# Kernel optimization log

Hardware: AMD Instinct MI355X
Metric: run time of the kernel (lower is better)

## Reference

```python
import jax, jax.numpy as jnp
import numpy as np
from jax.scipy.linalg import expm

DIM = 1024


def setup_inputs() -> dict:
    key = jax.random.key(0)
    k1, k2 = jax.random.split(key)
    x = jax.random.normal(k1, (4, 4096, DIM), dtype=jnp.float32)
    skew_weights = jax.random.normal(k2, (DIM, DIM), dtype=jnp.float32) * 0.01
    return {"x": x, "skew_weights": skew_weights}


def reference(x, skew_weights):
    # A is skew-symmetric -> expm(A) is a rotation in SO(dim)
    A = skew_weights - skew_weights.T          # [dim, dim]
    R = expm(A)                                # [dim, dim]
    return jnp.matmul(x, R)                    # [..., dim] @ [dim, dim]
```

## Files before the change

kernel.cpp:

```cpp
#include <hip/hip_runtime.h>
#include <stdint.h>

#define DIM 1024
#define GLOBAL_AS __attribute__((address_space(1)))
#define LDS_AS __attribute__((address_space(3)))

typedef short bf16x8 __attribute__((ext_vector_type(8)));
typedef float f32x4 __attribute__((ext_vector_type(4)));

#define C3 0.16666667f
#define C4 0.041666668f
#define C5 0.008333334f
#define C6 0.0013888889f
#define C7 1.9841270e-4f
#define C8 2.4801587e-5f

__device__ __forceinline__ unsigned short f32_to_bf16(float f) {
    union { float f; uint32_t u; } v; v.f = f;
    uint32_t u = v.u;
    u += 0x7FFFu + ((u >> 16) & 1u);
    return (unsigned short)(u >> 16);
}
__device__ __forceinline__ float bf16_to_f32(unsigned short u) {
    union { uint32_t u; float f; } v; v.u = ((uint32_t)u) << 16;
    return v.f;
}

__device__ __forceinline__ void async16(const void* g, void* l) {
    __builtin_amdgcn_global_load_lds((GLOBAL_AS const void*)g,
                                     (LDS_AS void*)l, 16, 0, 0);
}

__global__ __launch_bounds__(256) void k_init(const float* __restrict__ W,
        unsigned short* __restrict__ Ab, unsigned short* __restrict__ G) {
    int idx = blockIdx.x * 256 + threadIdx.x;
    int i = idx >> 10, j = idx & 1023;
    float a = W[i * DIM + j] - W[j * DIM + i];
    Ab[idx] = f32_to_bf16(a);
    G[idx]  = f32_to_bf16(-a);
}

__global__ __launch_bounds__(256) void k_convert(const float* __restrict__ X,
        unsigned short* __restrict__ Xb) {
    int id = blockIdx.x * 256 + threadIdx.x;
    const f32x4* p = (const f32x4*)(X + (size_t)id * 8);
    f32x4 v0 = p[0], v1 = p[1];
    unsigned short o[8];
    #pragma unroll
    for (int q = 0; q < 4; q++) { o[q] = f32_to_bf16(v0[q]); o[4 + q] = f32_to_bf16(v1[q]); }
    *(bf16x8*)&Xb[(size_t)id * 8] = *(bf16x8*)o;
}

template<int MODE>
__global__ __launch_bounds__(256) void k_pgemm(
        const unsigned short* __restrict__ P,
        const unsigned short* __restrict__ Qt,
        const unsigned short* __restrict__ Ab,
        const unsigned short* __restrict__ A2b,
        unsigned short* __restrict__ out1,
        unsigned short* __restrict__ out2) {
    __shared__ unsigned short lP[64 * 256];
    __shared__ unsigned short lQ[64 * 256];
    int tid = threadIdx.x;
    int m0 = blockIdx.y * 64, n0 = blockIdx.x * 64;
    int lane = tid & 63, w = tid >> 6;
    int wr = w >> 1, wc = w & 1;
    int rr = lane & 15, ko = lane >> 4;
    f32x4 acc[2][2] = {};
    for (int ks = 0; ks < 4; ks++) {
        int kb = ks * 256;
        #pragma unroll
        for (int i = 0; i < 8; i++) {
            int l = i * 256 + tid;
            int r = l >> 5, cst = l & 31;
            int cd = cst ^ (r & 7);
            async16(&P[(m0 + r) * DIM + kb + cd * 8], &lP[l * 8]);
            async16(&Qt[(n0 + r) * DIM + kb + cd * 8], &lQ[l * 8]);
        }
        __syncthreads();
        #pragma unroll
        for (int s = 0; s < 8; s++) {
            int cd = s * 4 + ko;
            bf16x8 af[2], bq[2];
            #pragma unroll
            for (int mi = 0; mi < 2; mi++) {
                int ra = wr * 32 + mi * 16 + rr;
                af[mi] = *(const bf16x8*)&lP[ra * 256 + ((cd ^ (ra & 7)) * 8)];
            }
            #pragma unroll
            for (int ni = 0; ni < 2; ni++) {
                int rb = wc * 32 + ni * 16 + rr;
                bq[ni] = *(const bf16x8*)&lQ[rb * 256 + ((cd ^ (rb & 7)) * 8)];
            }
            #pragma unroll
            for (int mi = 0; mi < 2; mi++)
                #pragma unroll
                for (int ni = 0; ni < 2; ni++)
                    acc[mi][ni] = __builtin_amdgcn_mfma_f32_16x16x32_bf16(
                        af[mi], bq[ni], acc[mi][ni], 0, 0, 0);
        }
        __syncthreads();
    }
    if (MODE == 1 || MODE == 2) {
        #pragma unroll
        for (int mi = 0; mi < 2; mi++)
            #pragma unroll
            for (int ni = 0; ni < 2; ni++)
                #pragma unroll
                for (int q = 0; q < 4; q++) {
                    int rl = wr * 32 + mi * 16 + ko * 4 + q;
                    int cl = wc * 32 + ni * 16 + rr;
                    int gi = (m0 + rl) * DIM + n0 + cl;
                    float v = acc[mi][ni][q];
                    out1[gi] = f32_to_bf16(v);
                    if (MODE == 1) {
                        float a = bf16_to_f32(Ab[gi]);
                        float d = (m0 + rl == n0 + cl) ? C6 : 0.0f;
                        out2[gi] = f32_to_bf16(d - C7 * a + C8 * v);
                    }
                }
    } else {
        float* tb = (float*)lP;
        #pragma unroll
        for (int mi = 0; mi < 2; mi++)
            #pragma unroll
            for (int ni = 0; ni < 2; ni++)
                #pragma unroll
                for (int q = 0; q < 4; q++) {
                    int rl = wr * 32 + mi * 16 + ko * 4 + q;
                    int cl = wc * 32 + ni * 16 + rr;
                    int gi = (m0 + rl) * DIM + n0 + cl;
                    float a = bf16_to_f32(Ab[gi]);
                    float a2 = bf16_to_f32(A2b[gi]);
                    float d = (m0 + rl == n0 + cl) ? 1.0f : 0.0f;
                    float v;
                    if (MODE == 3) v = acc[mi][ni][q] + C3 * d + C4 * a + C5 * a2;
                    else           v = acc[mi][ni][q] + d + a + 0.5f * a2;
                    tb[cl * 65 + rl] = v;
                }
        __syncthreads();
        #pragma unroll
        for (int q = 0; q < 16; q++) {
            int l = tid * 16 + q;
            int orow = l >> 6, ocol = l & 63;
            out1[(n0 + orow) * DIM + m0 + ocol] = f32_to_bf16(tb[orow * 65 + ocol]);
        }
    }
}

__global__ __launch_bounds__(256) void k_biggemm(
        const unsigned short* __restrict__ Xb,
        const unsigned short* __restrict__ Rtb,
        float* __restrict__ Out) {
    __shared__ unsigned short lX[128 * 32];
    __shared__ unsigned short lB[256 * 32];
    int tid = threadIdx.x;
    int bid = blockIdx.x;
    int m0 = (bid & 127) * 128, n0 = (bid >> 7) * 256;
    int lane = tid & 63, w = tid >> 6;
    int wr = w >> 1, wc = w & 1;
    int rr = lane & 15, ko = lane >> 4;
    f32x4 acc[4][8] = {};
    for (int kb = 0; kb < DIM; kb += 32) {
        #pragma unroll
        for (int i = 0; i < 2; i++) {
            int l = i * 256 + tid;
            int r = l >> 2, cst = l & 3;
            int cd = cst ^ ((r >> 1) & 3);
            async16(&Xb[(m0 + r) * DIM + kb + cd * 8], &lX[l * 8]);
        }
        #pragma unroll
        for (int i = 0; i < 4; i++) {
            int l = i * 256 + tid;
            int r = l >> 2, cst = l & 3;
            int cd = cst ^ ((r >> 1) & 3);
            async16(&Rtb[(n0 + r) * DIM + kb + cd * 8], &lB[l * 8]);
        }
        __syncthreads();
        bf16x8 af[4], bq[8];
        #pragma unroll
        for (int mi = 0; mi < 4; mi++) {
            int ra = wr * 64 + mi * 16 + rr;
            af[mi] = *(const bf16x8*)&lX[ra * 32 + ((ko ^ ((ra >> 1) & 3)) * 8)];
        }
        #pragma unroll
        for (int ni = 0; ni < 8; ni++) {
            int rb = wc * 128 + ni * 16 + rr;
            bq[ni] = *(const bf16x8*)&lB[rb * 32 + ((ko ^ ((rb >> 1) & 3)) * 8)];
        }
        #pragma unroll
        for (int mi = 0; mi < 4; mi++)
            #pragma unroll
            for (int ni = 0; ni < 8; ni++)
                acc[mi][ni] = __builtin_amdgcn_mfma_f32_16x16x32_bf16(
                    af[mi], bq[ni], acc[mi][ni], 0, 0, 0);
        __syncthreads();
    }
    #pragma unroll
    for (int mi = 0; mi < 4; mi++)
        #pragma unroll
        for (int ni = 0; ni < 8; ni++)
            #pragma unroll
            for (int q = 0; q < 4; q++) {
                int row = m0 + wr * 64 + mi * 16 + ko * 4 + q;
                int col = n0 + wc * 128 + ni * 16 + rr;
                Out[(size_t)row * DIM + col] = acc[mi][ni][q];
            }
}

__global__ __launch_bounds__(256) void k_biggemm_cvt(
        const float* __restrict__ X,
        const unsigned short* __restrict__ Rtb,
        float* __restrict__ Out) {
    __shared__ unsigned short lX[128 * 32];
    __shared__ unsigned short lB[256 * 32];
    int tid = threadIdx.x;
    int bid = blockIdx.x;
    int m0 = (bid & 127) * 128, n0 = (bid >> 7) * 256;
    int lane = tid & 63, w = tid >> 6;
    int wr = w >> 1, wc = w & 1;
    int rr = lane & 15, ko = lane >> 4;
    f32x4 acc[4][8] = {};
    int xr = tid >> 1, xh = tid & 1;
    int q3 = (xr >> 1) & 3;
    for (int kb = 0; kb < DIM; kb += 32) {
        {
            const float* xp = &X[(size_t)(m0 + xr) * DIM + kb + xh * 16];
            float xv[16];
            *(f32x4*)&xv[0] = *(const f32x4*)&xp[0];
            *(f32x4*)&xv[4] = *(const f32x4*)&xp[4];
            *(f32x4*)&xv[8] = *(const f32x4*)&xp[8];
            *(f32x4*)&xv[12] = *(const f32x4*)&xp[12];
            unsigned short xs[16];
            #pragma unroll
            for (int q = 0; q < 16; q++) xs[q] = f32_to_bf16(xv[q]);
            *(bf16x8*)&lX[xr * 32 + (((2 * xh) ^ q3) * 8)]     = *(bf16x8*)&xs[0];
            *(bf16x8*)&lX[xr * 32 + (((2 * xh + 1) ^ q3) * 8)] = *(bf16x8*)&xs[8];
        }
        #pragma unroll
        for (int i = 0; i < 4; i++) {
            int l = i * 256 + tid;
            int r = l >> 2, cst = l & 3;
            int cd = cst ^ ((r >> 1) & 3);
            async16(&Rtb[(n0 + r) * DIM + kb + cd * 8], &lB[l * 8]);
        }
        __syncthreads();
        bf16x8 af[4], bq[8];
        #pragma unroll
        for (int mi = 0; mi < 4; mi++) {
            int ra = wr * 64 + mi * 16 + rr;
            af[mi] = *(const bf16x8*)&lX[ra * 32 + ((ko ^ ((ra >> 1) & 3)) * 8)];
        }
        #pragma unroll
        for (int ni = 0; ni < 8; ni++) {
            int rb = wc * 128 + ni * 16 + rr;
            bq[ni] = *(const bf16x8*)&lB[rb * 32 + ((ko ^ ((rb >> 1) & 3)) * 8)];
        }
        #pragma unroll
        for (int mi = 0; mi < 4; mi++)
            #pragma unroll
            for (int ni = 0; ni < 8; ni++)
                acc[mi][ni] = __builtin_amdgcn_mfma_f32_16x16x32_bf16(
                    af[mi], bq[ni], acc[mi][ni], 0, 0, 0);
        __syncthreads();
    }
    #pragma unroll
    for (int mi = 0; mi < 4; mi++)
        #pragma unroll
        for (int ni = 0; ni < 8; ni++)
            #pragma unroll
            for (int q = 0; q < 4; q++) {
                int row = m0 + wr * 64 + mi * 16 + ko * 4 + q;
                int col = n0 + wc * 128 + ni * 16 + rr;
                Out[(size_t)row * DIM + col] = acc[mi][ni][q];
            }
}

extern "C" void kernel_launch(void* const* d_in, const int* in_sizes, int n_in,
                              void* d_out, int out_size, void* d_ws, size_t ws_size,
                              hipStream_t stream) {
    const float* X = (const float*)d_in[0];
    const float* W = (const float*)d_in[1];
    float* Out = (float*)d_out;
    char* ws = (char*)d_ws;
    const size_t MB = 1u << 20;
    unsigned short* Ab   = (unsigned short*)(ws + 0 * MB);
    unsigned short* G    = (unsigned short*)(ws + 2 * MB);
    unsigned short* A2b  = (unsigned short*)(ws + 4 * MB);
    unsigned short* A3b  = (unsigned short*)(ws + 6 * MB);
    unsigned short* B1tb = (unsigned short*)(ws + 8 * MB);
    unsigned short* B2tb = (unsigned short*)(ws + 10 * MB);
    unsigned short* Rtb  = (unsigned short*)(ws + 12 * MB);
    unsigned short* Xb   = (unsigned short*)(ws + 14 * MB);

    k_init<<<4096, 256, 0, stream>>>(W, Ab, G);
    k_pgemm<1><<<dim3(16, 16), 256, 0, stream>>>(Ab, G, Ab, nullptr, A2b, B1tb);
    k_pgemm<2><<<dim3(16, 16), 256, 0, stream>>>(Ab, A2b, nullptr, nullptr, A3b, nullptr);
    k_pgemm<3><<<dim3(16, 16), 256, 0, stream>>>(A3b, B1tb, Ab, A2b, B2tb, nullptr);
    k_pgemm<4><<<dim3(16, 16), 256, 0, stream>>>(A3b, B2tb, Ab, A2b, Rtb, nullptr);

    if (ws_size >= 46 * MB) {
        k_convert<<<8192, 256, 0, stream>>>(X, Xb);
        k_biggemm<<<512, 256, 0, stream>>>(Xb, Rtb, Out);
    } else {
        k_biggemm_cvt<<<512, 256, 0, stream>>>(X, Rtb, Out);
    }
}
```

Before: 199.1 us.

## Cut expm Taylor chain to 3 GEMMs, split-K pgemm, fuse fp32 X conversion into big GEMM

The matrix exponential polynomial drops the degree 7 and 8 terms, so R is built from three 1024x1024 GEMMs instead of four. Each small GEMM now runs 512 threads as two split-K groups whose partial sums are reduced through LDS, giving more parallelism to the 256-block grids. The main GEMM loads fp32 X straight into LDS asynchronously and converts it to bf16 in registers, which removes the separate convert kernel. Its tile shrinks to 128x128 across 1024 blocks. Truncating the series lowers accuracy, and the fp32 staging doubles the LDS traffic for X.

```diff
diff --git a/kernel.cpp b/kernel.cpp
--- a/kernel.cpp
+++ b/kernel.cpp
@@ -12,8 +12,6 @@
 #define C4 0.041666668f
 #define C5 0.008333334f
 #define C6 0.0013888889f
-#define C7 1.9841270e-4f
-#define C8 2.4801587e-5f
 
 __device__ __forceinline__ unsigned short f32_to_bf16(float f) {
     union { float f; uint32_t u; } v; v.f = f;
@@ -40,57 +38,50 @@
     G[idx]  = f32_to_bf16(-a);
 }
 
-__global__ __launch_bounds__(256) void k_convert(const float* __restrict__ X,
-        unsigned short* __restrict__ Xb) {
-    int id = blockIdx.x * 256 + threadIdx.x;
-    const f32x4* p = (const f32x4*)(X + (size_t)id * 8);
-    f32x4 v0 = p[0], v1 = p[1];
-    unsigned short o[8];
-    #pragma unroll
-    for (int q = 0; q < 4; q++) { o[q] = f32_to_bf16(v0[q]); o[4 + q] = f32_to_bf16(v1[q]); }
-    *(bf16x8*)&Xb[(size_t)id * 8] = *(bf16x8*)o;
-}
-
 template<int MODE>
-__global__ __launch_bounds__(256) void k_pgemm(
+__global__ __launch_bounds__(512) void k_pgemm(
         const unsigned short* __restrict__ P,
         const unsigned short* __restrict__ Qt,
         const unsigned short* __restrict__ Ab,
         const unsigned short* __restrict__ A2b,
         unsigned short* __restrict__ out1,
         unsigned short* __restrict__ out2) {
-    __shared__ unsigned short lP[64 * 256];
-    __shared__ unsigned short lQ[64 * 256];
+    __shared__ unsigned short lP[2][64 * 128];
+    __shared__ unsigned short lQ[2][64 * 128];
     int tid = threadIdx.x;
     int m0 = blockIdx.y * 64, n0 = blockIdx.x * 64;
-    int lane = tid & 63, w = tid >> 6;
-    int wr = w >> 1, wc = w & 1;
+    int g = tid >> 8;
+    int tg = tid & 255;
+    int lane = tid & 63;
+    int w4 = (tid >> 6) & 3;
+    int wr = w4 >> 1, wc = w4 & 1;
     int rr = lane & 15, ko = lane >> 4;
     f32x4 acc[2][2] = {};
+    int kbase = g * 512;
     for (int ks = 0; ks < 4; ks++) {
-        int kb = ks * 256;
-        #pragma unroll
-        for (int i = 0; i < 8; i++) {
-            int l = i * 256 + tid;
-            int r = l >> 5, cst = l & 31;
+        int kb = kbase + ks * 128;
+        #pragma unroll
+        for (int i = 0; i < 4; i++) {
+            int l = i * 256 + tg;
+            int r = l >> 4, cst = l & 15;
             int cd = cst ^ (r & 7);
-            async16(&P[(m0 + r) * DIM + kb + cd * 8], &lP[l * 8]);
-            async16(&Qt[(n0 + r) * DIM + kb + cd * 8], &lQ[l * 8]);
-        }
-        __syncthreads();
-        #pragma unroll
-        for (int s = 0; s < 8; s++) {
+            async16(&P[(m0 + r) * DIM + kb + cd * 8], &lP[g][l * 8]);
+            async16(&Qt[(n0 + r) * DIM + kb + cd * 8], &lQ[g][l * 8]);
+        }
+        __syncthreads();
+        #pragma unroll
+        for (int s = 0; s < 4; s++) {
             int cd = s * 4 + ko;
             bf16x8 af[2], bq[2];
             #pragma unroll
             for (int mi = 0; mi < 2; mi++) {
                 int ra = wr * 32 + mi * 16 + rr;
-                af[mi] = *(const bf16x8*)&lP[ra * 256 + ((cd ^ (ra & 7)) * 8)];
+                af[mi] = *(const bf16x8*)&lP[g][ra * 128 + ((cd ^ (ra & 7)) * 8)];
             }
             #pragma unroll
             for (int ni = 0; ni < 2; ni++) {
                 int rb = wc * 32 + ni * 16 + rr;
-                bq[ni] = *(const bf16x8*)&lQ[rb * 256 + ((cd ^ (rb & 7)) * 8)];
+                bq[ni] = *(const bf16x8*)&lQ[g][rb * 128 + ((cd ^ (rb & 7)) * 8)];
             }
             #pragma unroll
             for (int mi = 0; mi < 2; mi++)
@@ -101,97 +92,130 @@
         }
         __syncthreads();
     }
-    if (MODE == 1 || MODE == 2) {
+    float* rb = (float*)&lP[0][0];
+    if (g == 1) {
         #pragma unroll
         for (int mi = 0; mi < 2; mi++)
             #pragma unroll
             for (int ni = 0; ni < 2; ni++)
+                *(f32x4*)&rb[(w4 * 64 + lane) * 16 + (mi * 2 + ni) * 4] = acc[mi][ni];
+    }
+    __syncthreads();
+    if (g == 0) {
+        #pragma unroll
+        for (int mi = 0; mi < 2; mi++)
+            #pragma unroll
+            for (int ni = 0; ni < 2; ni++)
+                acc[mi][ni] += *(const f32x4*)&rb[(w4 * 64 + lane) * 16 + (mi * 2 + ni) * 4];
+        if (MODE == 1 || MODE == 2) {
+            #pragma unroll
+            for (int mi = 0; mi < 2; mi++)
                 #pragma unroll
-                for (int q = 0; q < 4; q++) {
-                    int rl = wr * 32 + mi * 16 + ko * 4 + q;
-                    int cl = wc * 32 + ni * 16 + rr;
-                    int gi = (m0 + rl) * DIM + n0 + cl;
-                    float v = acc[mi][ni][q];
-                    out1[gi] = f32_to_bf16(v);
-                    if (MODE == 1) {
+                for (int ni = 0; ni < 2; ni++)
+                    #pragma unroll
+                    for (int q = 0; q < 4; q++) {
+                        int rl = wr * 32 + mi * 16 + ko * 4 + q;
+                        int cl = wc * 32 + ni * 16 + rr;
+                        int gi = (m0 + rl) * DIM + n0 + cl;
+                        float v = acc[mi][ni][q];
+                        out1[gi] = f32_to_bf16(v);
+                        if (MODE == 2) {
+                            float a = bf16_to_f32(Ab[gi]);
+                            float a2 = bf16_to_f32(A2b[gi]);
+                            float d = (m0 + rl == n0 + cl) ? C3 : 0.0f;
+                            out2[gi] = f32_to_bf16(d - C4 * a + C5 * a2 - C6 * v);
+                        }
+                    }
+        } else {
+            float* tb = (float*)&lQ[0][0];
+            #pragma unroll
+            for (int mi = 0; mi < 2; mi++)
+                #pragma unroll
+                for (int ni = 0; ni < 2; ni++)
+                    #pragma unroll
+                    for (int q = 0; q < 4; q++) {
+                        int rl = wr * 32 + mi * 16 + ko * 4 + q;
+                        int cl = wc * 32 + ni * 16 + rr;
+                        int gi = (m0 + rl) * DIM + n0 + cl;
                         float a = bf16_to_f32(Ab[gi]);
-                        float d = (m0 + rl == n0 + cl) ? C6 : 0.0f;
-                        out2[gi] = f32_to_bf16(d - C7 * a + C8 * v);
+                        float a2 = bf16_to_f32(A2b[gi]);
+                        float d = (m0 + rl == n0 + cl) ? 1.0f : 0.0f;
+                        tb[cl * 65 + rl] = acc[mi][ni][q] + d + a + 0.5f * a2;
                     }
-                }
-    } else {
-        float* tb = (float*)lP;
-        #pragma unroll
-        for (int mi = 0; mi < 2; mi++)
-            #pragma unroll
-            for (int ni = 0; ni < 2; ni++)
-                #pragma unroll
-                for (int q = 0; q < 4; q++) {
-                    int rl = wr * 32 + mi * 16 + ko * 4 + q;
-                    int cl = wc * 32 + ni * 16 + rr;
-                    int gi = (m0 + rl) * DIM + n0 + cl;
-                    float a = bf16_to_f32(Ab[gi]);
-                    float a2 = bf16_to_f32(A2b[gi]);
-                    float d = (m0 + rl == n0 + cl) ? 1.0f : 0.0f;
-                    float v;
-                    if (MODE == 3) v = acc[mi][ni][q] + C3 * d + C4 * a + C5 * a2;
-                    else           v = acc[mi][ni][q] + d + a + 0.5f * a2;
-                    tb[cl * 65 + rl] = v;
-                }
-        __syncthreads();
-        #pragma unroll
-        for (int q = 0; q < 16; q++) {
-            int l = tid * 16 + q;
-            int orow = l >> 6, ocol = l & 63;
-            out1[(n0 + orow) * DIM + m0 + ocol] = f32_to_bf16(tb[orow * 65 + ocol]);
+        }
+    }
+    if (MODE == 3) {
+        __syncthreads();
+        if (g == 0) {
+            const float* tb = (const float*)&lQ[0][0];
+            #pragma unroll
+            for (int q = 0; q < 16; q++) {
+                int l = tg * 16 + q;
+                int orow = l >> 6, ocol = l & 63;
+                out1[(n0 + orow) * DIM + m0 + ocol] = f32_to_bf16(tb[orow * 65 + ocol]);
+            }
         }
     }
 }
 
 __global__ __launch_bounds__(256) void k_biggemm(
-        const unsigned short* __restrict__ Xb,
+        const float* __restrict__ X,
         const unsigned short* __restrict__ Rtb,
         float* __restrict__ Out) {
-    __shared__ unsigned short lX[128 * 32];
-    __shared__ unsigned short lB[256 * 32];
+    __shared__ float lX[128 * 32];
+    __shared__ unsigned short lB[128 * 32];
     int tid = threadIdx.x;
     int bid = blockIdx.x;
-    int m0 = (bid & 127) * 128, n0 = (bid >> 7) * 256;
+    int m0 = (bid & 127) * 128, n0 = (bid >> 7) * 128;
     int lane = tid & 63, w = tid >> 6;
     int wr = w >> 1, wc = w & 1;
     int rr = lane & 15, ko = lane >> 4;
-    f32x4 acc[4][8] = {};
+    f32x4 acc[4][4] = {};
     for (int kb = 0; kb < DIM; kb += 32) {
+        #pragma unroll
+        for (int i = 0; i < 4; i++) {
+            int l = i * 256 + tid;
+            int r = l >> 3, cst = l & 7;
+            int cd = cst ^ (r & 7);
+            async16(&X[(size_t)(m0 + r) * DIM + kb + cd * 4], &lX[l * 4]);
+        }
         #pragma unroll
         for (int i = 0; i < 2; i++) {
             int l = i * 256 + tid;
             int r = l >> 2, cst = l & 3;
             int cd = cst ^ ((r >> 1) & 3);
-            async16(&Xb[(m0 + r) * DIM + kb + cd * 8], &lX[l * 8]);
-        }
-        #pragma unroll
-        for (int i = 0; i < 4; i++) {
-            int l = i * 256 + tid;
-            int r = l >> 2, cst = l & 3;
-            int cd = cst ^ ((r >> 1) & 3);
             async16(&Rtb[(n0 + r) * DIM + kb + cd * 8], &lB[l * 8]);
         }
         __syncthreads();
-        bf16x8 af[4], bq[8];
+        bf16x8 af[4], bq[4];
         #pragma unroll
         for (int mi = 0; mi < 4; mi++) {
             int ra = wr * 64 + mi * 16 + rr;
-            af[mi] = *(const bf16x8*)&lX[ra * 32 + ((ko ^ ((ra >> 1) & 3)) * 8)];
-        }
-        #pragma unroll
-        for (int ni = 0; ni < 8; ni++) {
-            int rb = wc * 128 + ni * 16 + rr;
+            int s0 = (2 * ko) ^ (ra & 7);
+            int s1 = (2 * ko + 1) ^ (ra & 7);
+            union { f32x4 f; uint32_t u[4]; } a0, a1;
+            a0.f = *(const f32x4*)&lX[ra * 32 + s0 * 4];
+            a1.f = *(const f32x4*)&lX[ra * 32 + s1 * 4];
+            union { uint32_t u[4]; bf16x8 v; } pk;
+            uint32_t b0 = a0.u[0] + 0x8000u, b1 = a0.u[1] + 0x8000u;
+            uint32_t b2 = a0.u[2] + 0x8000u, b3 = a0.u[3] + 0x8000u;
+            uint32_t b4 = a1.u[0] + 0x8000u, b5 = a1.u[1] + 0x8000u;
+            uint32_t b6 = a1.u[2] + 0x8000u, b7 = a1.u[3] + 0x8000u;
+            pk.u[0] = __builtin_amdgcn_perm(b1, b0, 0x07060302u);
+            pk.u[1] = __builtin_amdgcn_perm(b3, b2, 0x07060302u);
+            pk.u[2] = __builtin_amdgcn_perm(b5, b4, 0x07060302u);
+            pk.u[3] = __builtin_amdgcn_perm(b7, b6, 0x07060302u);
+            af[mi] = pk.v;
+        }
+        #pragma unroll
+        for (int ni = 0; ni < 4; ni++) {
+            int rb = wc * 64 + ni * 16 + rr;
             bq[ni] = *(const bf16x8*)&lB[rb * 32 + ((ko ^ ((rb >> 1) & 3)) * 8)];
         }
         #pragma unroll
         for (int mi = 0; mi < 4; mi++)
             #pragma unroll
-            for (int ni = 0; ni < 8; ni++)
+            for (int ni = 0; ni < 4; ni++)
                 acc[mi][ni] = __builtin_amdgcn_mfma_f32_16x16x32_bf16(
                     af[mi], bq[ni], acc[mi][ni], 0, 0, 0);
         __syncthreads();
@@ -199,79 +223,11 @@
     #pragma unroll
     for (int mi = 0; mi < 4; mi++)
         #pragma unroll
-        for (int ni = 0; ni < 8; ni++)
+        for (int ni = 0; ni < 4; ni++)
             #pragma unroll
             for (int q = 0; q < 4; q++) {
                 int row = m0 + wr * 64 + mi * 16 + ko * 4 + q;
-                int col = n0 + wc * 128 + ni * 16 + rr;
-                Out[(size_t)row * DIM + col] = acc[mi][ni][q];
-            }
-}
-
-__global__ __launch_bounds__(256) void k_biggemm_cvt(
-        const float* __restrict__ X,
-        const unsigned short* __restrict__ Rtb,
-        float* __restrict__ Out) {
-    __shared__ unsigned short lX[128 * 32];
-    __shared__ unsigned short lB[256 * 32];
-    int tid = threadIdx.x;
-    int bid = blockIdx.x;
-    int m0 = (bid & 127) * 128, n0 = (bid >> 7) * 256;
-    int lane = tid & 63, w = tid >> 6;
-    int wr = w >> 1, wc = w & 1;
-    int rr = lane & 15, ko = lane >> 4;
-    f32x4 acc[4][8] = {};
-    int xr = tid >> 1, xh = tid & 1;
-    int q3 = (xr >> 1) & 3;
-    for (int kb = 0; kb < DIM; kb += 32) {
-        {
-            const float* xp = &X[(size_t)(m0 + xr) * DIM + kb + xh * 16];
-            float xv[16];
-            *(f32x4*)&xv[0] = *(const f32x4*)&xp[0];
-            *(f32x4*)&xv[4] = *(const f32x4*)&xp[4];
-            *(f32x4*)&xv[8] = *(const f32x4*)&xp[8];
-            *(f32x4*)&xv[12] = *(const f32x4*)&xp[12];
-            unsigned short xs[16];
-            #pragma unroll
-            for (int q = 0; q < 16; q++) xs[q] = f32_to_bf16(xv[q]);
-            *(bf16x8*)&lX[xr * 32 + (((2 * xh) ^ q3) * 8)]     = *(bf16x8*)&xs[0];
-            *(bf16x8*)&lX[xr * 32 + (((2 * xh + 1) ^ q3) * 8)] = *(bf16x8*)&xs[8];
-        }
-        #pragma unroll
-        for (int i = 0; i < 4; i++) {
-            int l = i * 256 + tid;
-            int r = l >> 2, cst = l & 3;
-            int cd = cst ^ ((r >> 1) & 3);
-            async16(&Rtb[(n0 + r) * DIM + kb + cd * 8], &lB[l * 8]);
-        }
-        __syncthreads();
-        bf16x8 af[4], bq[8];
-        #pragma unroll
-        for (int mi = 0; mi < 4; mi++) {
-            int ra = wr * 64 + mi * 16 + rr;
-            af[mi] = *(const bf16x8*)&lX[ra * 32 + ((ko ^ ((ra >> 1) & 3)) * 8)];
-        }
-        #pragma unroll
-        for (int ni = 0; ni < 8; ni++) {
-            int rb = wc * 128 + ni * 16 + rr;
-            bq[ni] = *(const bf16x8*)&lB[rb * 32 + ((ko ^ ((rb >> 1) & 3)) * 8)];
-        }
-        #pragma unroll
-        for (int mi = 0; mi < 4; mi++)
-            #pragma unroll
-            for (int ni = 0; ni < 8; ni++)
-                acc[mi][ni] = __builtin_amdgcn_mfma_f32_16x16x32_bf16(
-                    af[mi], bq[ni], acc[mi][ni], 0, 0, 0);
-        __syncthreads();
-    }
-    #pragma unroll
-    for (int mi = 0; mi < 4; mi++)
-        #pragma unroll
-        for (int ni = 0; ni < 8; ni++)
-            #pragma unroll
-            for (int q = 0; q < 4; q++) {
-                int row = m0 + wr * 64 + mi * 16 + ko * 4 + q;
-                int col = n0 + wc * 128 + ni * 16 + rr;
+                int col = n0 + wc * 64 + ni * 16 + rr;
                 Out[(size_t)row * DIM + col] = acc[mi][ni][q];
             }
 }
@@ -284,25 +240,16 @@
     float* Out = (float*)d_out;
     char* ws = (char*)d_ws;
     const size_t MB = 1u << 20;
-    unsigned short* Ab   = (unsigned short*)(ws + 0 * MB);
-    unsigned short* G    = (unsigned short*)(ws + 2 * MB);
-    unsigned short* A2b  = (unsigned short*)(ws + 4 * MB);
-    unsigned short* A3b  = (unsigned short*)(ws + 6 * MB);
-    unsigned short* B1tb = (unsigned short*)(ws + 8 * MB);
-    unsigned short* B2tb = (unsigned short*)(ws + 10 * MB);
-    unsigned short* Rtb  = (unsigned short*)(ws + 12 * MB);
-    unsigned short* Xb   = (unsigned short*)(ws + 14 * MB);
+    unsigned short* Ab  = (unsigned short*)(ws + 0 * MB);
+    unsigned short* G   = (unsigned short*)(ws + 2 * MB);
+    unsigned short* A2b = (unsigned short*)(ws + 4 * MB);
+    unsigned short* A3b = (unsigned short*)(ws + 6 * MB);
+    unsigned short* Qtb = (unsigned short*)(ws + 8 * MB);
+    unsigned short* Rtb = (unsigned short*)(ws + 10 * MB);
 
     k_init<<<4096, 256, 0, stream>>>(W, Ab, G);
-    k_pgemm<1><<<dim3(16, 16), 256, 0, stream>>>(Ab, G, Ab, nullptr, A2b, B1tb);
-    k_pgemm<2><<<dim3(16, 16), 256, 0, stream>>>(Ab, A2b, nullptr, nullptr, A3b, nullptr);
-    k_pgemm<3><<<dim3(16, 16), 256, 0, stream>>>(A3b, B1tb, Ab, A2b, B2tb, nullptr);
-    k_pgemm<4><<<dim3(16, 16), 256, 0, stream>>>(A3b, B2tb, Ab, A2b, Rtb, nullptr);
-
-    if (ws_size >= 46 * MB) {
-        k_convert<<<8192, 256, 0, stream>>>(X, Xb);
-        k_biggemm<<<512, 256, 0, stream>>>(Xb, Rtb, Out);
-    } else {
-        k_biggemm_cvt<<<512, 256, 0, stream>>>(X, Rtb, Out);
-    }
-}
+    k_pgemm<1><<<dim3(16, 16), 512, 0, stream>>>(Ab, G,   Ab, nullptr, A2b, nullptr);
+    k_pgemm<2><<<dim3(16, 16), 512, 0, stream>>>(Ab, A2b, Ab, A2b,     A3b, Qtb);
+    k_pgemm<3><<<dim3(16, 16), 512, 0, stream>>>(A3b, Qtb, Ab, A2b,    Rtb, nullptr);
+    k_biggemm<<<1024, 256, 0, stream>>>(X, Rtb, Out);
+}
```

Result: slower. 206.3 us (+3.6%).
